# Kernel optimization log

Measured on AMD Instinct MI355X. Metric: run time of the kernel, lower is better.

Reference implementation:

```python
import jax, jax.numpy as jnp
import numpy as np

N_ATOMS = 512
B = 14            # orbitals per atom (basis block size)
F = 128           # node feature dim
FE = 128          # edge feature dim
HID = 256
P = N_ATOMS * (N_ATOMS - 1) // 2


def setup_inputs() -> dict:
    key = jax.random.key(0)
    ks = jax.random.split(key, 12)
    s = 0.02  # small init scale for MLP weights
    pi, pj = jnp.triu_indices(N_ATOMS, k=1)
    return {
        "nodes_feature": jax.random.normal(ks[0], (N_ATOMS, F), jnp.float32),
        "edges_feature": jax.random.normal(ks[1], (N_ATOMS, N_ATOMS, FE), jnp.float32),
        "atom_blocks": jax.random.normal(ks[2], (N_ATOMS, B, B), jnp.float32),
        "overlap_pair": jax.random.normal(ks[3], (P, B, B), jnp.float32),
        "W1": jax.random.normal(ks[4], (F + FE, HID), jnp.float32) * s,
        "b1": jnp.zeros((HID,), jnp.float32),
        "W2": jax.random.normal(ks[5], (HID, B * B), jnp.float32) * s,
        "b2": jnp.zeros((B * B,), jnp.float32),
        "Wo1": jax.random.normal(ks[6], (2 * F + FE, HID), jnp.float32) * s,
        "bo1": jnp.zeros((HID,), jnp.float32),
        "Wo2": jax.random.normal(ks[7], (HID, B * B), jnp.float32) * s,
        "bo2": jnp.zeros((B * B,), jnp.float32),
        "pair_i": pi.astype(jnp.int32),
        "pair_j": pj.astype(jnp.int32),
    }


def reference(nodes_feature, edges_feature, atom_blocks, overlap_pair,
              W1, b1, W2, b2, Wo1, bo1, Wo2, bo2, pair_i, pair_j):
    n = nodes_feature.shape[0]
    ar = jnp.arange(n)

    # ---- diagonal blocks: MLP(node_i, edge_ii) -> BxB correction of atom block
    e_ii = edges_feature[ar, ar]                          # [N, FE]
    x = jnp.concatenate([nodes_feature, e_ii], axis=-1)   # [N, F+FE]
    h = jax.nn.silu(x @ W1 + b1)
    m = (h @ W2 + b2).reshape(n, B, B)
    diag_blocks = atom_blocks + m                         # [N, B, B]

    # ---- off-diagonal blocks: MLP(node_i, node_j, edge_ij) -> BxB correction
    ni = nodes_feature[pair_i]                            # [P, F]
    nj = nodes_feature[pair_j]                            # [P, F]
    eij = edges_feature[pair_i, pair_j]                   # [P, FE]
    xo = jnp.concatenate([ni, nj, eij], axis=-1)          # [P, 2F+FE]
    ho = jax.nn.silu(xo @ Wo1 + bo1)
    mo = (ho @ Wo2 + bo2).reshape(-1, B, B)
    off_blocks = overlap_pair + mo                        # [P, B, B]

    # ---- scatter blocks into dense Hamiltonian [N*B, N*B]
    Hm = jnp.zeros((n, B, n, B), dtype=nodes_feature.dtype)
    Hm = Hm.at[ar, :, ar, :].set(diag_blocks)
    Hm = Hm.at[pair_i, :, pair_j, :].set(off_blocks)
    Hm = Hm.at[pair_j, :, pair_i, :].set(jnp.transpose(off_blocks, (0, 2, 1)))
    return Hm.reshape(n * B, n * B)
```

## Files before the change

kernel.cpp:

```cpp
#include <hip/hip_runtime.h>
#include <stdint.h>

typedef unsigned short u16;
typedef unsigned int u32;
typedef __bf16 bf16x8 __attribute__((ext_vector_type(8)));
typedef float f32x4 __attribute__((ext_vector_type(4)));

#define N_ATOMS 512
#define BDIM 14
#define BB 196
#define FDIM 128
#define HROW 7168
#define NPAIR 130816
#define NPBLK (NPAIR / 128)

#define OFF_W1F   0
#define OFF_W2F   65536
#define OFF_WO1F  118784
#define OFF_WO2F  217088
#define WS_ELEMS  270336

__device__ __forceinline__ float b2f(u16 u) {
    union { u32 u; float f; } c; c.u = ((u32)u) << 16; return c.f;
}
__device__ __forceinline__ u16 fb(float f) {
    union { float f; u32 u; } c; c.f = f;
    u32 r = c.u + 0x7fff + ((c.u >> 16) & 1);
    return (u16)(r >> 16);
}
__device__ __forceinline__ bf16x8 ld16b(const u16* p) {
    return *(const bf16x8*)(const void*)p;
}
__device__ __forceinline__ bf16x8 ldcvt8(const float* p) {
    const float4 a = *(const float4*)(const void*)p;
    const float4 b = *(const float4*)(const void*)(p + 4);
    bf16x8 r;
    r[0] = (__bf16)a.x; r[1] = (__bf16)a.y; r[2] = (__bf16)a.z; r[3] = (__bf16)a.w;
    r[4] = (__bf16)b.x; r[5] = (__bf16)b.y; r[6] = (__bf16)b.z; r[7] = (__bf16)b.w;
    return r;
}

__global__ void prep_kernel(const float* __restrict__ W1, const float* __restrict__ W2,
                            const float* __restrict__ Wo1, const float* __restrict__ Wo2,
                            u16* __restrict__ ws) {
    int gid = blockIdx.x * 256 + threadIdx.x;
    const float* src; int idx, NT, Ncols, Nreal;
    if (gid < OFF_W2F)       { idx = gid;             src = W1;  NT = 16; Ncols = 256; Nreal = 256; }
    else if (gid < OFF_WO1F) { idx = gid - OFF_W2F;   src = W2;  NT = 13; Ncols = 196; Nreal = 196; }
    else if (gid < OFF_WO2F) { idx = gid - OFF_WO1F;  src = Wo1; NT = 16; Ncols = 256; Nreal = 256; }
    else                     { idx = gid - OFF_WO2F;  src = Wo2; NT = 13; Ncols = 196; Nreal = 196; }
    int jj   = idx & 7;
    int lane = (idx >> 3) & 63;
    int tile = idx >> 9;
    int nt = tile % NT;
    int ks = tile / NT;
    int k = ks * 32 + ((lane >> 4) << 3) + jj;
    int n = nt * 16 + (lane & 15);
    ws[gid] = (n < Nreal) ? fb(src[k * Ncols + n]) : (u16)0;
}

__global__ __launch_bounds__(256, 2)
void ham_main(const float* __restrict__ nodes, const float* __restrict__ edges,
              const float* __restrict__ atomb, const float* __restrict__ ovl,
              const float* __restrict__ b1v, const float* __restrict__ b2v,
              const float* __restrict__ bo1, const float* __restrict__ bo2,
              const int* __restrict__ pair_i, const int* __restrict__ pair_j,
              const u16* __restrict__ ws, float* __restrict__ out)
{
    __shared__ u16 sH[128 * 264];
    __shared__ int sI[128], sJ[128];
    const int tid = threadIdx.x;
    const int w = tid >> 6, lane = tid & 63;
    const int q = lane >> 4, l15 = lane & 15;
    const int bid = blockIdx.x;
    const bool isPair = bid < NPBLK;
    const int wr = w >> 1, wc = w & 1;

    const float* rowA[4];
    const float* rowB[4];
    const float* rowE[4];
    int KS1;
    const u16 *WAf, *WBf;
    const float *bias1, *bias2;

    if (isPair) {
        const int pbase = bid * 128;
        KS1 = 12; WAf = ws + OFF_WO1F; WBf = ws + OFF_WO2F; bias1 = bo1; bias2 = bo2;
        if (tid < 128) { int p = pbase + tid; sI[tid] = pair_i[p]; sJ[tid] = pair_j[p]; }
        #pragma unroll
        for (int pp = 0; pp < 4; ++pp) {
            int p = pbase + wc * 64 + pp * 16 + l15;
            int i = pair_i[p], j = pair_j[p];
            rowA[pp] = nodes + (size_t)i * FDIM;
            rowB[pp] = nodes + (size_t)j * FDIM;
            rowE[pp] = edges + ((size_t)i * N_ATOMS + j) * FDIM;
        }
    } else {
        const int nbase = (bid - NPBLK) * 128;
        KS1 = 8; WAf = ws + OFF_W1F; WBf = ws + OFF_W2F; bias1 = b1v; bias2 = b2v;
        #pragma unroll
        for (int pp = 0; pp < 4; ++pp) {
            int nn = nbase + wc * 64 + pp * 16 + l15;
            rowA[pp] = nodes + (size_t)nn * FDIM;
            rowB[pp] = edges + ((size_t)nn * N_ATOMS + nn) * FDIM;
            rowE[pp] = rowB[pp];
        }
    }

    f32x4 acc[8][4];
    #pragma unroll
    for (int a = 0; a < 8; ++a)
        #pragma unroll
        for (int b = 0; b < 4; ++b)
            acc[a][b] = (f32x4){0.f, 0.f, 0.f, 0.f};

    for (int ks = 0; ks < KS1; ++ks) {
        const int seg = ks >> 2;
        const int koff = (ks & 3) * 32 + q * 8;
        bf16x8 bfr[4];
        #pragma unroll
        for (int pp = 0; pp < 4; ++pp) {
            const float* base = (seg == 0) ? rowA[pp] : (seg == 1) ? rowB[pp] : rowE[pp];
            bfr[pp] = ldcvt8(base + koff);
        }
        const u16* ap = WAf + ((size_t)((ks * 16 + wr * 8) * 64 + lane)) * 8;
        #pragma unroll
        for (int hh = 0; hh < 8; ++hh) {
            bf16x8 afr = ld16b(ap + (size_t)hh * 512);
            #pragma unroll
            for (int pp = 0; pp < 4; ++pp)
                acc[hh][pp] = __builtin_amdgcn_mfma_f32_16x16x32_bf16(afr, bfr[pp], acc[hh][pp], 0, 0, 0);
        }
    }

    #pragma unroll
    for (int hh = 0; hh < 8; ++hh) {
        const int h0 = wr * 128 + hh * 16 + q * 4;
        const float bb0 = bias1[h0], bb1 = bias1[h0 + 1];
        const float bb2 = bias1[h0 + 2], bb3 = bias1[h0 + 3];
        #pragma unroll
        for (int pp = 0; pp < 4; ++pp) {
            const int row = wc * 64 + pp * 16 + l15;
            float x0 = acc[hh][pp][0] + bb0, x1 = acc[hh][pp][1] + bb1;
            float x2 = acc[hh][pp][2] + bb2, x3 = acc[hh][pp][3] + bb3;
            float s0 = x0 / (1.f + __expf(-x0)), s1 = x1 / (1.f + __expf(-x1));
            float s2 = x2 / (1.f + __expf(-x2)), s3 = x3 / (1.f + __expf(-x3));
            uint2 pk;
            pk.x = (u32)fb(s0) | ((u32)fb(s1) << 16);
            pk.y = (u32)fb(s2) | ((u32)fb(s3) << 16);
            *(uint2*)(void*)&sH[row * 264 + h0] = pk;
        }
    }
    __syncthreads();

    f32x4 acc2[2][13];
    #pragma unroll
    for (int m = 0; m < 2; ++m)
        #pragma unroll
        for (int n = 0; n < 13; ++n)
            acc2[m][n] = (f32x4){0.f, 0.f, 0.f, 0.f};

    for (int ks = 0; ks < 8; ++ks) {
        bf16x8 a2[2];
        #pragma unroll
        for (int mm = 0; mm < 2; ++mm) {
            const int row = w * 32 + mm * 16 + l15;
            a2[mm] = ld16b(&sH[row * 264 + ks * 32 + q * 8]);
        }
        const u16* bp = WBf + ((size_t)((ks * 13) * 64 + lane)) * 8;
        #pragma unroll
        for (int nt = 0; nt < 13; ++nt) {
            bf16x8 bfr = ld16b(bp + (size_t)nt * 512);
            acc2[0][nt] = __builtin_amdgcn_mfma_f32_16x16x32_bf16(a2[0], bfr, acc2[0][nt], 0, 0, 0);
            acc2[1][nt] = __builtin_amdgcn_mfma_f32_16x16x32_bf16(a2[1], bfr, acc2[1][nt], 0, 0, 0);
        }
    }
    __syncthreads();

    u16* sOut = sH;
    #pragma unroll
    for (int nt = 0; nt < 13; ++nt) {
        const int e = nt * 16 + l15;
        if (e < BB) {
            const float be = bias2[e];
            #pragma unroll
            for (int mm = 0; mm < 2; ++mm) {
                const int pr = w * 32 + mm * 16 + q * 4;
                #pragma unroll
                for (int r = 0; r < 4; ++r)
                    sOut[(pr + r) * BB + e] = fb(acc2[mm][nt][r] + be);
            }
        }
    }
    __syncthreads();

    if (isPair) {
        const int pbase = bid * 128;
        const float* src = ovl + (size_t)pbase * BB;
        for (int idx = tid; idx < 12544; idx += 256) {
            const int off = idx * 2;
            const float2 a = *(const float2*)(const void*)(src + off);
            u32 h = *(u32*)(void*)(sOut + off);
            float lo = b2f((u16)h) + a.x;
            float hi = b2f((u16)(h >> 16)) + a.y;
            *(u32*)(void*)(sOut + off) = (u32)fb(lo) | ((u32)fb(hi) << 16);
        }
        __syncthreads();
        for (int u = tid; u < 12544; u += 256) {
            const int a = u / 896;
            const int r = u - a * 896;
            const int pl = r / 7;
            const int c2 = (r - pl * 7) * 2;
            const int i = sI[pl], j = sJ[pl];
            u32 v = *(const u32*)(const void*)(sOut + pl * BB + a * 14 + c2);
            float2 o; o.x = b2f((u16)v); o.y = b2f((u16)(v >> 16));
            size_t addr = (size_t)(i * 14 + a) * HROW + j * 14 + c2;
            *(float2*)(void*)(out + addr) = o;
        }
        for (int u = tid; u < 12544; u += 256) {
            const int pl = u / 98;
            const int r = u - pl * 98;
            const int b = r / 7;
            const int a2i = (r - b * 7) * 2;
            const int i = sI[pl], j = sJ[pl];
            float2 o;
            o.x = b2f(sOut[pl * BB + a2i * 14 + b]);
            o.y = b2f(sOut[pl * BB + (a2i + 1) * 14 + b]);
            size_t addr = (size_t)(j * 14 + b) * HROW + i * 14 + a2i;
            *(float2*)(void*)(out + addr) = o;
        }
    } else {
        const int nbase = (bid - NPBLK) * 128;
        const float* src = atomb + (size_t)nbase * BB;
        for (int idx = tid; idx < 12544; idx += 256) {
            const int off = idx * 2;
            const float2 a = *(const float2*)(const void*)(src + off);
            u32 h = *(u32*)(void*)(sOut + off);
            float lo = b2f((u16)h) + a.x;
            float hi = b2f((u16)(h >> 16)) + a.y;
            *(u32*)(void*)(sOut + off) = (u32)fb(lo) | ((u32)fb(hi) << 16);
        }
        __syncthreads();
        for (int u = tid; u < 12544; u += 256) {
            const int a = u / 896;
            const int r = u - a * 896;
            const int pl = r / 7;
            const int c2 = (r - pl * 7) * 2;
            const int nn = nbase + pl;
            u32 v = *(const u32*)(const void*)(sOut + pl * BB + a * 14 + c2);
            float2 o; o.x = b2f((u16)v); o.y = b2f((u16)(v >> 16));
            size_t addr = (size_t)(nn * 14 + a) * HROW + nn * 14 + c2;
            *(float2*)(void*)(out + addr) = o;
        }
    }
}

extern "C" void kernel_launch(void* const* d_in, const int* in_sizes, int n_in,
                              void* d_out, int out_size, void* d_ws, size_t ws_size,
                              hipStream_t stream) {
    const float* nodes = (const float*)d_in[0];
    const float* edges = (const float*)d_in[1];
    const float* atomb = (const float*)d_in[2];
    const float* ovl   = (const float*)d_in[3];
    const float* W1    = (const float*)d_in[4];
    const float* b1    = (const float*)d_in[5];
    const float* W2    = (const float*)d_in[6];
    const float* b2    = (const float*)d_in[7];
    const float* Wo1   = (const float*)d_in[8];
    const float* bo1   = (const float*)d_in[9];
    const float* Wo2   = (const float*)d_in[10];
    const float* bo2   = (const float*)d_in[11];
    const int* pi      = (const int*)d_in[12];
    const int* pj      = (const int*)d_in[13];
    u16* ws    = (u16*)d_ws;
    float* out = (float*)d_out;

    prep_kernel<<<WS_ELEMS / 256, 256, 0, stream>>>(W1, W2, Wo1, Wo2, ws);
    ham_main<<<NPBLK + N_ATOMS / 128, 256, 0, stream>>>(nodes, edges, atomb, ovl,
                                                        b1, b2, bo1, bo2, pi, pj, ws, out);
}
```

Measured before the change: 519.8 us.

## Halve rows per block, raise occupancy, fuse residual add into epilogue

Each block now handles 64 rows instead of 128, so each wave covers 64 hidden columns and 16 output rows, with fewer accumulator registers. Launch bounds move to 4 blocks per SM. The overlap/atom-block residual is added directly during the second GEMM epilogue, which removes a separate shared-memory pass and one barrier. Pointer arrays become 32-bit offsets to save registers. The trade-off is that weight fragments are reloaded across twice as many blocks, and the residual loads in the epilogue are strided rather than coalesced.

```diff
diff --git a/kernel.cpp b/kernel.cpp
--- a/kernel.cpp
+++ b/kernel.cpp
@@ -12,7 +12,10 @@
 #define FDIM 128
 #define HROW 7168
 #define NPAIR 130816
-#define NPBLK (NPAIR / 128)
+#define ROWS 64
+#define NPBLK (NPAIR / ROWS)
+#define NBLK  (NPBLK + N_ATOMS / ROWS)
+#define HALFU (ROWS * BB / 2)
 
 #define OFF_W1F   0
 #define OFF_W2F   65536
@@ -59,7 +62,7 @@
     ws[gid] = (n < Nreal) ? fb(src[k * Ncols + n]) : (u16)0;
 }
 
-__global__ __launch_bounds__(256, 2)
+__global__ __launch_bounds__(256, 4)
 void ham_main(const float* __restrict__ nodes, const float* __restrict__ edges,
               const float* __restrict__ atomb, const float* __restrict__ ovl,
               const float* __restrict__ b1v, const float* __restrict__ b2v,
@@ -67,49 +70,49 @@
               const int* __restrict__ pair_i, const int* __restrict__ pair_j,
               const u16* __restrict__ ws, float* __restrict__ out)
 {
-    __shared__ u16 sH[128 * 264];
-    __shared__ int sI[128], sJ[128];
+    __shared__ u16 sH[ROWS * 264];
+    __shared__ int sI[ROWS], sJ[ROWS];
     const int tid = threadIdx.x;
     const int w = tid >> 6, lane = tid & 63;
     const int q = lane >> 4, l15 = lane & 15;
     const int bid = blockIdx.x;
     const bool isPair = bid < NPBLK;
-    const int wr = w >> 1, wc = w & 1;
-
-    const float* rowA[4];
-    const float* rowB[4];
-    const float* rowE[4];
+
+    u32 offA[4], offB[4], offE[4];
     int KS1;
     const u16 *WAf, *WBf;
     const float *bias1, *bias2;
+    const float *seg1base;
 
     if (isPair) {
-        const int pbase = bid * 128;
+        const int pbase = bid * ROWS;
         KS1 = 12; WAf = ws + OFF_WO1F; WBf = ws + OFF_WO2F; bias1 = bo1; bias2 = bo2;
-        if (tid < 128) { int p = pbase + tid; sI[tid] = pair_i[p]; sJ[tid] = pair_j[p]; }
-        #pragma unroll
-        for (int pp = 0; pp < 4; ++pp) {
-            int p = pbase + wc * 64 + pp * 16 + l15;
+        seg1base = nodes;
+        if (tid < ROWS) { int p = pbase + tid; sI[tid] = pair_i[p]; sJ[tid] = pair_j[p]; }
+        #pragma unroll
+        for (int pp = 0; pp < 4; ++pp) {
+            int p = pbase + pp * 16 + l15;
             int i = pair_i[p], j = pair_j[p];
-            rowA[pp] = nodes + (size_t)i * FDIM;
-            rowB[pp] = nodes + (size_t)j * FDIM;
-            rowE[pp] = edges + ((size_t)i * N_ATOMS + j) * FDIM;
+            offA[pp] = (u32)i * FDIM;
+            offB[pp] = (u32)j * FDIM;
+            offE[pp] = ((u32)i * N_ATOMS + (u32)j) * FDIM;
         }
     } else {
-        const int nbase = (bid - NPBLK) * 128;
+        const int nbase = (bid - NPBLK) * ROWS;
         KS1 = 8; WAf = ws + OFF_W1F; WBf = ws + OFF_W2F; bias1 = b1v; bias2 = b2v;
-        #pragma unroll
-        for (int pp = 0; pp < 4; ++pp) {
-            int nn = nbase + wc * 64 + pp * 16 + l15;
-            rowA[pp] = nodes + (size_t)nn * FDIM;
-            rowB[pp] = edges + ((size_t)nn * N_ATOMS + nn) * FDIM;
-            rowE[pp] = rowB[pp];
-        }
-    }
-
-    f32x4 acc[8][4];
-    #pragma unroll
-    for (int a = 0; a < 8; ++a)
+        seg1base = edges;
+        #pragma unroll
+        for (int pp = 0; pp < 4; ++pp) {
+            int nn = nbase + pp * 16 + l15;
+            offA[pp] = (u32)nn * FDIM;
+            offB[pp] = ((u32)nn * N_ATOMS + (u32)nn) * FDIM;
+            offE[pp] = offB[pp];
+        }
+    }
+
+    f32x4 acc[4][4];
+    #pragma unroll
+    for (int a = 0; a < 4; ++a)
         #pragma unroll
         for (int b = 0; b < 4; ++b)
             acc[a][b] = (f32x4){0.f, 0.f, 0.f, 0.f};
@@ -117,15 +120,16 @@
     for (int ks = 0; ks < KS1; ++ks) {
         const int seg = ks >> 2;
         const int koff = (ks & 3) * 32 + q * 8;
+        const float* bse = (seg == 0) ? nodes : (seg == 1) ? seg1base : edges;
         bf16x8 bfr[4];
         #pragma unroll
         for (int pp = 0; pp < 4; ++pp) {
-            const float* base = (seg == 0) ? rowA[pp] : (seg == 1) ? rowB[pp] : rowE[pp];
-            bfr[pp] = ldcvt8(base + koff);
-        }
-        const u16* ap = WAf + ((size_t)((ks * 16 + wr * 8) * 64 + lane)) * 8;
-        #pragma unroll
-        for (int hh = 0; hh < 8; ++hh) {
+            const u32 off = (seg == 0) ? offA[pp] : (seg == 1) ? offB[pp] : offE[pp];
+            bfr[pp] = ldcvt8(bse + off + koff);
+        }
+        const u16* ap = WAf + ((size_t)((ks * 16 + w * 4) * 64 + lane)) * 8;
+        #pragma unroll
+        for (int hh = 0; hh < 4; ++hh) {
             bf16x8 afr = ld16b(ap + (size_t)hh * 512);
             #pragma unroll
             for (int pp = 0; pp < 4; ++pp)
@@ -134,13 +138,13 @@
     }
 
     #pragma unroll
-    for (int hh = 0; hh < 8; ++hh) {
-        const int h0 = wr * 128 + hh * 16 + q * 4;
+    for (int hh = 0; hh < 4; ++hh) {
+        const int h0 = w * 64 + hh * 16 + q * 4;
         const float bb0 = bias1[h0], bb1 = bias1[h0 + 1];
         const float bb2 = bias1[h0 + 2], bb3 = bias1[h0 + 3];
         #pragma unroll
         for (int pp = 0; pp < 4; ++pp) {
-            const int row = wc * 64 + pp * 16 + l15;
+            const int row = pp * 16 + l15;
             float x0 = acc[hh][pp][0] + bb0, x1 = acc[hh][pp][1] + bb1;
             float x2 = acc[hh][pp][2] + bb2, x3 = acc[hh][pp][3] + bb3;
             float s0 = x0 / (1.f + __expf(-x0)), s1 = x1 / (1.f + __expf(-x1));
@@ -153,62 +157,45 @@
     }
     __syncthreads();
 
-    f32x4 acc2[2][13];
-    #pragma unroll
-    for (int m = 0; m < 2; ++m)
-        #pragma unroll
-        for (int n = 0; n < 13; ++n)
-            acc2[m][n] = (f32x4){0.f, 0.f, 0.f, 0.f};
-
+    f32x4 acc2[13];
+    #pragma unroll
+    for (int n = 0; n < 13; ++n)
+        acc2[n] = (f32x4){0.f, 0.f, 0.f, 0.f};
+
+    const int row2 = w * 16 + l15;
     for (int ks = 0; ks < 8; ++ks) {
-        bf16x8 a2[2];
-        #pragma unroll
-        for (int mm = 0; mm < 2; ++mm) {
-            const int row = w * 32 + mm * 16 + l15;
-            a2[mm] = ld16b(&sH[row * 264 + ks * 32 + q * 8]);
-        }
+        bf16x8 a2 = ld16b(&sH[row2 * 264 + ks * 32 + q * 8]);
         const u16* bp = WBf + ((size_t)((ks * 13) * 64 + lane)) * 8;
         #pragma unroll
         for (int nt = 0; nt < 13; ++nt) {
             bf16x8 bfr = ld16b(bp + (size_t)nt * 512);
-            acc2[0][nt] = __builtin_amdgcn_mfma_f32_16x16x32_bf16(a2[0], bfr, acc2[0][nt], 0, 0, 0);
-            acc2[1][nt] = __builtin_amdgcn_mfma_f32_16x16x32_bf16(a2[1], bfr, acc2[1][nt], 0, 0, 0);
+            acc2[nt] = __builtin_amdgcn_mfma_f32_16x16x32_bf16(a2, bfr, acc2[nt], 0, 0, 0);
         }
     }
     __syncthreads();
 
     u16* sOut = sH;
+    const float* addsrc = isPair ? (ovl + (size_t)bid * ROWS * BB)
+                                 : (atomb + (size_t)(bid - NPBLK) * ROWS * BB);
+    const int pr = w * 16 + q * 4;
     #pragma unroll
     for (int nt = 0; nt < 13; ++nt) {
         const int e = nt * 16 + l15;
         if (e < BB) {
             const float be = bias2[e];
             #pragma unroll
-            for (int mm = 0; mm < 2; ++mm) {
-                const int pr = w * 32 + mm * 16 + q * 4;
-                #pragma unroll
-                for (int r = 0; r < 4; ++r)
-                    sOut[(pr + r) * BB + e] = fb(acc2[mm][nt][r] + be);
+            for (int r = 0; r < 4; ++r) {
+                float v = acc2[nt][r] + be + addsrc[(size_t)(pr + r) * BB + e];
+                sOut[(pr + r) * BB + e] = fb(v);
             }
         }
     }
     __syncthreads();
 
     if (isPair) {
-        const int pbase = bid * 128;
-        const float* src = ovl + (size_t)pbase * BB;
-        for (int idx = tid; idx < 12544; idx += 256) {
-            const int off = idx * 2;
-            const float2 a = *(const float2*)(const void*)(src + off);
-            u32 h = *(u32*)(void*)(sOut + off);
-            float lo = b2f((u16)h) + a.x;
-            float hi = b2f((u16)(h >> 16)) + a.y;
-            *(u32*)(void*)(sOut + off) = (u32)fb(lo) | ((u32)fb(hi) << 16);
-        }
-        __syncthreads();
-        for (int u = tid; u < 12544; u += 256) {
-            const int a = u / 896;
-            const int r = u - a * 896;
+        for (int u = tid; u < HALFU; u += 256) {
+            const int a = u / 448;
+            const int r = u - a * 448;
             const int pl = r / 7;
             const int c2 = (r - pl * 7) * 2;
             const int i = sI[pl], j = sJ[pl];
@@ -217,7 +204,7 @@
             size_t addr = (size_t)(i * 14 + a) * HROW + j * 14 + c2;
             *(float2*)(void*)(out + addr) = o;
         }
-        for (int u = tid; u < 12544; u += 256) {
+        for (int u = tid; u < HALFU; u += 256) {
             const int pl = u / 98;
             const int r = u - pl * 98;
             const int b = r / 7;
@@ -230,20 +217,10 @@
             *(float2*)(void*)(out + addr) = o;
         }
     } else {
-        const int nbase = (bid - NPBLK) * 128;
-        const float* src = atomb + (size_t)nbase * BB;
-        for (int idx = tid; idx < 12544; idx += 256) {
-            const int off = idx * 2;
-            const float2 a = *(const float2*)(const void*)(src + off);
-            u32 h = *(u32*)(void*)(sOut + off);
-            float lo = b2f((u16)h) + a.x;
-            float hi = b2f((u16)(h >> 16)) + a.y;
-            *(u32*)(void*)(sOut + off) = (u32)fb(lo) | ((u32)fb(hi) << 16);
-        }
-        __syncthreads();
-        for (int u = tid; u < 12544; u += 256) {
-            const int a = u / 896;
-            const int r = u - a * 896;
+        const int nbase = (bid - NPBLK) * ROWS;
+        for (int u = tid; u < HALFU; u += 256) {
+            const int a = u / 448;
+            const int r = u - a * 448;
             const int pl = r / 7;
             const int c2 = (r - pl * 7) * 2;
             const int nn = nbase + pl;
@@ -276,6 +253,6 @@
     float* out = (float*)d_out;
 
     prep_kernel<<<WS_ELEMS / 256, 256, 0, stream>>>(W1, W2, Wo1, Wo2, ws);
-    ham_main<<<NPBLK + N_ATOMS / 128, 256, 0, stream>>>(nodes, edges, atomb, ovl,
-                                                        b1, b2, bo1, bo2, pi, pj, ws, out);
-}
+    ham_main<<<NBLK, 256, 0, stream>>>(nodes, edges, atomb, ovl,
+                                       b1, b2, bo1, bo2, pi, pj, ws, out);
+}
```

New measurement: 518.6 us. About the same (-0.2%).
